# Kernel optimization log

Measured on AMD Instinct MI355X. Metric: run time of the kernel, lower is better.

## Reference

```python
import jax, jax.numpy as jnp
import numpy as np

N = 100000   # num variables
D_IN = 512
D_OUT = 512
C = 4096     # num clusters
K = 32       # vars per cluster
E = 16384    # cluster edges
S = 16       # shared vars per edge
H = 4        # num heads
NEG_SLOPE = 0.2


def setup_inputs() -> dict:
    key = jax.random.key(0)
    ks = jax.random.split(key, 8)
    xav = (6.0 / (D_IN + D_OUT)) ** 0.5  # xavier_uniform bound
    x_var = jax.random.normal(ks[0], (N, D_IN), dtype=jnp.float32)
    W_Q = jax.random.uniform(ks[1], (D_OUT, D_IN), jnp.float32, -xav, xav)
    W_K = jax.random.uniform(ks[2], (D_OUT, D_IN), jnp.float32, -xav, xav)
    W_V = jax.random.uniform(ks[3], (D_OUT, D_IN), jnp.float32, -xav, xav)
    head_weights = jnp.ones((H,), jnp.float32)
    cluster_var_ids = jax.random.randint(ks[4], (C, K), 0, N)
    cluster_edge_index = jax.random.randint(ks[5], (2, E), 0, C)
    shared_vars = jax.random.randint(ks[6], (E, S), 0, N)
    return {
        'x_var': x_var, 'W_Q': W_Q, 'W_K': W_K, 'W_V': W_V,
        'head_weights': head_weights,
        'cluster_var_ids': cluster_var_ids,
        'cluster_edge_index': cluster_edge_index,
        'shared_vars': shared_vars,
        'active_heads': 4,
    }


def reference(x_var, W_Q, W_K, W_V, head_weights,
              cluster_var_ids, cluster_edge_index, shared_vars, active_heads):
    # Per-cluster mean pooling over member variables: [C, D_in]
    cluster_feats = x_var[cluster_var_ids].mean(axis=1)
    # Linear projections (torch Linear: y = x @ W.T)
    Q = cluster_feats @ W_Q.T   # [C, D_out]
    Kc = cluster_feats @ W_K.T  # [C, D_out]
    V = cluster_feats @ W_V.T   # [C, D_out]
    c1 = cluster_edge_index[0]  # [E] source clusters
    c2 = cluster_edge_index[1]  # [E] target clusters
    # Scalar dot-product attention per cluster edge
    scale = jnp.asarray(D_OUT, jnp.float32) ** 0.5
    scores = jnp.einsum('ed,ed->e', Q[c1], Kc[c2]) / scale
    scores = jnp.where(scores >= 0, scores, NEG_SLOPE * scores)  # leaky_relu
    attn = jax.nn.sigmoid(scores) * head_weights[:active_heads].mean()  # [E]
    # Per-edge message = attn * V[c2], broadcast to each shared var of the edge
    upd = attn[:, None] * V[c2]                                   # [E, D_out]
    upd_flat = jnp.broadcast_to(upd[:, None, :], (E, S, D_OUT)).reshape(E * S, D_OUT)
    x_out = x_var.at[shared_vars.reshape(-1)].add(upd_flat)
    return x_out
```

## Files before the change

### kernel.cpp

```cpp
#include <hip/hip_runtime.h>
#include <hip/hip_bf16.h>
#include <math.h>

#define N_VARS    100000
#define D_DIM     512
#define C_CLUST   4096
#define K_VARS    32
#define E_EDGES   16384
#define S_SHARED  16
#define H_HEADS   4
#define CAP       32
#define NEG_SLOPE 0.2f

typedef __bf16 bf16x8_t __attribute__((ext_vector_type(8)));
typedef float  f32x4_t  __attribute__((ext_vector_type(4)));

__device__ __forceinline__ unsigned int f32_to_bf16_bits(float f) {
    unsigned int u = __builtin_bit_cast(unsigned int, f);
    unsigned int lsb = (u >> 16) & 1u;
    u += 0x7fffu + lsb;
    return u >> 16;
}
__device__ __forceinline__ unsigned int pack_bf16x2(float a, float b) {
    return (f32_to_bf16_bits(b) << 16) | f32_to_bf16_bits(a);
}
__device__ __forceinline__ float bf16_bits_to_f32(unsigned int h) {
    unsigned int u = h << 16;
    return __builtin_bit_cast(float, u);
}

__device__ __forceinline__ int decode_active_heads(const int* p) {
    int raw = p[0];
    if (raw >= 1 && raw <= H_HEADS) return raw;
    float f = __builtin_bit_cast(float, raw);
    if (f >= 1.0f && f <= (float)H_HEADS) return (int)f;
    return H_HEADS;
}

__global__ void convert_w_kernel(const float* __restrict__ Wq,
                                 const float* __restrict__ Wk,
                                 const float* __restrict__ Wv,
                                 unsigned int* __restrict__ Wb) {
    const float* W = (blockIdx.y == 0) ? Wq : (blockIdx.y == 1) ? Wk : Wv;
    int i = blockIdx.x * blockDim.x + threadIdx.x;
    float2 w = ((const float2*)W)[i];
    Wb[(size_t)blockIdx.y * (D_DIM * D_DIM / 2) + i] = pack_bf16x2(w.x, w.y);
}

__global__ void pool_kernel(const float* __restrict__ x,
                            const int* __restrict__ cvid,
                            uint2* __restrict__ cfb ) {
    int c = blockIdx.x * 2 + (threadIdx.x >> 7);
    int t = threadIdx.x & 127;
    float4 acc = {0.f, 0.f, 0.f, 0.f};
#pragma unroll 4
    for (int k = 0; k < K_VARS; ++k) {
        int v = cvid[c * K_VARS + k];
        float4 w = ((const float4*)(x + (size_t)v * D_DIM))[t];
        acc.x += w.x; acc.y += w.y; acc.z += w.z; acc.w += w.w;
    }
    const float inv = 1.0f / (float)K_VARS;
    uint2 o;
    o.x = pack_bf16x2(acc.x * inv, acc.y * inv);
    o.y = pack_bf16x2(acc.z * inv, acc.w * inv);
    cfb[(size_t)c * (D_DIM / 4) + t] = o;
}

__global__ __launch_bounds__(256) void gemm_kernel(
        const unsigned short* __restrict__ cfb,
        const unsigned short* __restrict__ Wb,
        float* __restrict__ Qo, float* __restrict__ Ko, float* __restrict__ Vo) {
    const unsigned short* W = Wb + (size_t)blockIdx.z * D_DIM * D_DIM;
    float* O = (blockIdx.z == 0) ? Qo : (blockIdx.z == 1) ? Ko : Vo;

    int wave = threadIdx.x >> 6;
    int lane = threadIdx.x & 63;
    int m0 = blockIdx.x * 64 + wave * 16;
    int n0 = blockIdx.y * 64;
    int mr = m0 + (lane & 15);
    int kb = (lane >> 4) * 8;

    f32x4_t acc0 = {0.f,0.f,0.f,0.f}, acc1 = {0.f,0.f,0.f,0.f};
    f32x4_t acc2 = {0.f,0.f,0.f,0.f}, acc3 = {0.f,0.f,0.f,0.f};
    const unsigned short* arow = cfb + (size_t)mr * D_DIM + kb;
    const unsigned short* b0r  = W + (size_t)(n0 +  0 + (lane & 15)) * D_DIM + kb;
    const unsigned short* b1r  = W + (size_t)(n0 + 16 + (lane & 15)) * D_DIM + kb;
    const unsigned short* b2r  = W + (size_t)(n0 + 32 + (lane & 15)) * D_DIM + kb;
    const unsigned short* b3r  = W + (size_t)(n0 + 48 + (lane & 15)) * D_DIM + kb;
#pragma unroll 4
    for (int k0 = 0; k0 < D_DIM; k0 += 32) {
        bf16x8_t a  = *(const bf16x8_t*)(arow + k0);
        bf16x8_t b0 = *(const bf16x8_t*)(b0r + k0);
        bf16x8_t b1 = *(const bf16x8_t*)(b1r + k0);
        bf16x8_t b2 = *(const bf16x8_t*)(b2r + k0);
        bf16x8_t b3 = *(const bf16x8_t*)(b3r + k0);
        acc0 = __builtin_amdgcn_mfma_f32_16x16x32_bf16(a, b0, acc0, 0, 0, 0);
        acc1 = __builtin_amdgcn_mfma_f32_16x16x32_bf16(a, b1, acc1, 0, 0, 0);
        acc2 = __builtin_amdgcn_mfma_f32_16x16x32_bf16(a, b2, acc2, 0, 0, 0);
        acc3 = __builtin_amdgcn_mfma_f32_16x16x32_bf16(a, b3, acc3, 0, 0, 0);
    }
    int rb = m0 + (lane >> 4) * 4;
    int cl = lane & 15;
#pragma unroll
    for (int r = 0; r < 4; ++r) {
        float* orow = O + (size_t)(rb + r) * D_DIM + n0 + cl;
        orow[ 0] = acc0[r];
        orow[16] = acc1[r];
        orow[32] = acc2[r];
        orow[48] = acc3[r];
    }
}

__global__ void score_kernel(const float* __restrict__ Q,
                             const float* __restrict__ Kc,
                             const int* __restrict__ cei,
                             const float* __restrict__ hw,
                             const int* __restrict__ active_heads,
                             float* __restrict__ attn) {
    int e = blockIdx.x * 4 + (threadIdx.x >> 6);
    int lane = threadIdx.x & 63;
    int c1 = cei[e];
    int c2 = cei[E_EDGES + e];
    const float4* q = (const float4*)(Q  + (size_t)c1 * D_DIM);
    const float4* k = (const float4*)(Kc + (size_t)c2 * D_DIM);
    float4 qa = q[lane], qb = q[lane + 64];
    float4 ka = k[lane], kb = k[lane + 64];
    float s = qa.x*ka.x + qa.y*ka.y + qa.z*ka.z + qa.w*ka.w
            + qb.x*kb.x + qb.y*kb.y + qb.z*kb.z + qb.w*kb.w;
#pragma unroll
    for (int off = 32; off > 0; off >>= 1)
        s += __shfl_xor(s, off);
    if (lane == 0) {
        int ah = decode_active_heads(active_heads);
        float m = 0.f;
        for (int h = 0; h < ah; ++h) m += hw[h];
        m /= (float)ah;
        float sc = s * (1.0f / sqrtf((float)D_DIM));
        sc = sc >= 0.f ? sc : NEG_SLOPE * sc;
        attn[e] = m / (1.f + __expf(-sc));
    }
}

__global__ void fill_kernel(const int* __restrict__ shared_vars,
                            const int* __restrict__ cei,
                            const float* __restrict__ attn,
                            int* __restrict__ counts,
                            unsigned int* __restrict__ bucket) {
    int j = blockIdx.x * blockDim.x + threadIdx.x;
    if (j >= E_EDGES * S_SHARED) return;
    int v = shared_vars[j];
    int e = j >> 4;
    int pos = atomicAdd(&counts[v], 1);
    if (pos < CAP) {
        unsigned int packed = (f32_to_bf16_bits(attn[e]) << 16) | (unsigned int)cei[E_EDGES + e];
        bucket[(size_t)v * CAP + pos] = packed;
    }
}

__global__ void gather_kernel(const float* __restrict__ x,
                              const float* __restrict__ V,
                              const int* __restrict__ counts,
                              const unsigned int* __restrict__ bucket,
                              float* __restrict__ out) {
    int v = blockIdx.x * 2 + (threadIdx.x >> 7);
    int t = threadIdx.x & 127;
    float4 a = ((const float4*)(x + (size_t)v * D_DIM))[t];
    int cnt = counts[v];
    if (cnt > CAP) cnt = CAP;
    const unsigned int* bk = bucket + (size_t)v * CAP;
    for (int k = 0; k < cnt; ++k) {
        unsigned int pw = bk[k];
        float at = bf16_bits_to_f32(pw >> 16);
        int c2 = pw & 0xFFFu;
        float4 vv = ((const float4*)(V + (size_t)c2 * D_DIM))[t];
        a.x += at * vv.x; a.y += at * vv.y; a.z += at * vv.z; a.w += at * vv.w;
    }
    ((float4*)(out + (size_t)v * D_DIM))[t] = a;
}

extern "C" void kernel_launch(void* const* d_in, const int* in_sizes, int n_in,
                              void* d_out, int out_size, void* d_ws, size_t ws_size,
                              hipStream_t stream) {
    const float* x_var = (const float*)d_in[0];
    const float* W_Q   = (const float*)d_in[1];
    const float* W_K   = (const float*)d_in[2];
    const float* W_V   = (const float*)d_in[3];
    const float* hw    = (const float*)d_in[4];
    const int* cvid  = (const int*)d_in[5];
    const int* cei   = (const int*)d_in[6];
    const int* shv   = (const int*)d_in[7];
    const int* ahp   = (const int*)d_in[8];

    char* ws = (char*)d_ws;
    const size_t MiB = 1024 * 1024;
    unsigned int* cfb = (unsigned int*)(ws + 0);
    unsigned int* Wb  = (unsigned int*)(ws + 4  * MiB);
    float* Q    = (float*)(ws + 6  * MiB);
    float* Kc   = (float*)(ws + 14 * MiB);
    float* V    = (float*)(ws + 22 * MiB);
    float* attn = (float*)(ws + 30 * MiB);
    int* counts = (int*)(ws + 30 * MiB + 65536);
    unsigned int* bucket = (unsigned int*)(ws + 31 * MiB);

    convert_w_kernel<<<dim3(D_DIM * D_DIM / 2 / 256, 3), 256, 0, stream>>>(
        W_Q, W_K, W_V, Wb);

    pool_kernel<<<C_CLUST / 2, 256, 0, stream>>>(x_var, cvid, (uint2*)cfb);

    gemm_kernel<<<dim3(C_CLUST / 64, D_DIM / 64, 3), 256, 0, stream>>>(
        (const unsigned short*)cfb, (const unsigned short*)Wb, Q, Kc, V);

    score_kernel<<<E_EDGES / 4, 256, 0, stream>>>(Q, Kc, cei, hw, ahp, attn);

    hipMemsetAsync(counts, 0, (size_t)N_VARS * sizeof(int), stream);
    fill_kernel<<<(E_EDGES * S_SHARED + 255) / 256, 256, 0, stream>>>(
        shv, cei, attn, counts, bucket);

    gather_kernel<<<N_VARS / 2, 256, 0, stream>>>(x_var, V, counts, bucket,
                                                  (float*)d_out);
}
```

Baseline: 530.9 us.

## Fuse score with bucket fill, zero counts in pool, widen gather per wave

Merges the score and fill kernels so each edge's attention is computed and scattered into per-variable buckets in one pass, dropping the attn buffer and one launch. The counts memset moves into the pool kernel, and the pool loop is unrolled further with a scalarised cluster index. Gather now assigns one wave per variable, loads four bucket entries at once and issues up to four V-row loads before accumulating, with nontemporal output stores. The bucket read as uint4 relies on 16-byte alignment and reads past cnt within the CAP-sized slot.

Result: faster. 495.4 us (-6.7%).

```diff
diff --git a/kernel.cpp b/kernel.cpp
--- a/kernel.cpp
+++ b/kernel.cpp
@@ -49,13 +49,19 @@
 
 __global__ void pool_kernel(const float* __restrict__ x,
                             const int* __restrict__ cvid,
-                            uint2* __restrict__ cfb ) {
+                            uint2* __restrict__ cfb ,
+                            int* __restrict__ counts) {
+    int gtid = blockIdx.x * blockDim.x + threadIdx.x;
+    if (gtid < N_VARS) counts[gtid] = 0;
+
     int c = blockIdx.x * 2 + (threadIdx.x >> 7);
+    c = __builtin_amdgcn_readfirstlane(c);
     int t = threadIdx.x & 127;
+    const int* cv = cvid + c * K_VARS;
     float4 acc = {0.f, 0.f, 0.f, 0.f};
-#pragma unroll 4
+#pragma unroll 8
     for (int k = 0; k < K_VARS; ++k) {
-        int v = cvid[c * K_VARS + k];
+        int v = cv[k];
         float4 w = ((const float4*)(x + (size_t)v * D_DIM))[t];
         acc.x += w.x; acc.y += w.y; acc.z += w.z; acc.w += w.w;
     }
@@ -111,13 +117,16 @@
     }
 }
 
-__global__ void score_kernel(const float* __restrict__ Q,
-                             const float* __restrict__ Kc,
-                             const int* __restrict__ cei,
-                             const float* __restrict__ hw,
-                             const int* __restrict__ active_heads,
-                             float* __restrict__ attn) {
-    int e = blockIdx.x * 4 + (threadIdx.x >> 6);
+__global__ __launch_bounds__(256) void score_fill_kernel(
+        const float* __restrict__ Q,
+        const float* __restrict__ Kc,
+        const int* __restrict__ cei,
+        const float* __restrict__ hw,
+        const int* __restrict__ active_heads,
+        const int* __restrict__ shared_vars,
+        int* __restrict__ counts,
+        unsigned int* __restrict__ bucket) {
+    int e = __builtin_amdgcn_readfirstlane(blockIdx.x * 4 + (threadIdx.x >> 6));
     int lane = threadIdx.x & 63;
     int c1 = cei[e];
     int c2 = cei[E_EDGES + e];
@@ -130,52 +139,62 @@
 #pragma unroll
     for (int off = 32; off > 0; off >>= 1)
         s += __shfl_xor(s, off);
-    if (lane == 0) {
-        int ah = decode_active_heads(active_heads);
-        float m = 0.f;
-        for (int h = 0; h < ah; ++h) m += hw[h];
-        m /= (float)ah;
-        float sc = s * (1.0f / sqrtf((float)D_DIM));
-        sc = sc >= 0.f ? sc : NEG_SLOPE * sc;
-        attn[e] = m / (1.f + __expf(-sc));
-    }
-}
-
-__global__ void fill_kernel(const int* __restrict__ shared_vars,
-                            const int* __restrict__ cei,
-                            const float* __restrict__ attn,
-                            int* __restrict__ counts,
-                            unsigned int* __restrict__ bucket) {
-    int j = blockIdx.x * blockDim.x + threadIdx.x;
-    if (j >= E_EDGES * S_SHARED) return;
-    int v = shared_vars[j];
-    int e = j >> 4;
-    int pos = atomicAdd(&counts[v], 1);
-    if (pos < CAP) {
-        unsigned int packed = (f32_to_bf16_bits(attn[e]) << 16) | (unsigned int)cei[E_EDGES + e];
-        bucket[(size_t)v * CAP + pos] = packed;
-    }
-}
-
-__global__ void gather_kernel(const float* __restrict__ x,
-                              const float* __restrict__ V,
-                              const int* __restrict__ counts,
-                              const unsigned int* __restrict__ bucket,
-                              float* __restrict__ out) {
-    int v = blockIdx.x * 2 + (threadIdx.x >> 7);
-    int t = threadIdx.x & 127;
-    float4 a = ((const float4*)(x + (size_t)v * D_DIM))[t];
+    int ah = decode_active_heads(active_heads);
+    float m = 0.f;
+    for (int h = 0; h < ah; ++h) m += hw[h];
+    m /= (float)ah;
+    float sc = s * (1.0f / sqrtf((float)D_DIM));
+    sc = sc >= 0.f ? sc : NEG_SLOPE * sc;
+    float attn = m / (1.f + __expf(-sc));
+    unsigned int packed = (f32_to_bf16_bits(attn) << 16) | (unsigned int)c2;
+    if (lane < S_SHARED) {
+        int v = shared_vars[e * S_SHARED + lane];
+        int pos = atomicAdd(&counts[v], 1);
+        if (pos < CAP) bucket[(size_t)v * CAP + pos] = packed;
+    }
+}
+
+__global__ __launch_bounds__(256) void gather_kernel(
+        const float* __restrict__ x,
+        const float* __restrict__ V,
+        const int* __restrict__ counts,
+        const unsigned int* __restrict__ bucket,
+        float* __restrict__ out) {
+    int v = __builtin_amdgcn_readfirstlane(blockIdx.x * 4 + (threadIdx.x >> 6));
+    int lane = threadIdx.x & 63;
+    const f32x4_t* xr = (const f32x4_t*)(x + (size_t)v * D_DIM);
+    f32x4_t a0 = xr[lane];
+    f32x4_t a1 = xr[lane + 64];
     int cnt = counts[v];
     if (cnt > CAP) cnt = CAP;
     const unsigned int* bk = bucket + (size_t)v * CAP;
-    for (int k = 0; k < cnt; ++k) {
-        unsigned int pw = bk[k];
-        float at = bf16_bits_to_f32(pw >> 16);
-        int c2 = pw & 0xFFFu;
-        float4 vv = ((const float4*)(V + (size_t)c2 * D_DIM))[t];
-        a.x += at * vv.x; a.y += at * vv.y; a.z += at * vv.z; a.w += at * vv.w;
-    }
-    ((float4*)(out + (size_t)v * D_DIM))[t] = a;
+    for (int k = 0; k < cnt; k += 4) {
+        uint4 pw = *(const uint4*)(bk + k);
+        int m = cnt - k;
+        const f32x4_t* r0 = (const f32x4_t*)(V + (size_t)(pw.x & 0xFFFu) * D_DIM);
+        f32x4_t u0a = r0[lane], u0b = r0[lane + 64];
+        f32x4_t u1a, u1b, u2a, u2b, u3a, u3b;
+        if (m > 1) {
+            const f32x4_t* r1 = (const f32x4_t*)(V + (size_t)(pw.y & 0xFFFu) * D_DIM);
+            u1a = r1[lane]; u1b = r1[lane + 64];
+        }
+        if (m > 2) {
+            const f32x4_t* r2 = (const f32x4_t*)(V + (size_t)(pw.z & 0xFFFu) * D_DIM);
+            u2a = r2[lane]; u2b = r2[lane + 64];
+        }
+        if (m > 3) {
+            const f32x4_t* r3 = (const f32x4_t*)(V + (size_t)(pw.w & 0xFFFu) * D_DIM);
+            u3a = r3[lane]; u3b = r3[lane + 64];
+        }
+        float t0 = bf16_bits_to_f32(pw.x >> 16);
+        a0 += t0 * u0a; a1 += t0 * u0b;
+        if (m > 1) { float t1 = bf16_bits_to_f32(pw.y >> 16); a0 += t1 * u1a; a1 += t1 * u1b; }
+        if (m > 2) { float t2 = bf16_bits_to_f32(pw.z >> 16); a0 += t2 * u2a; a1 += t2 * u2b; }
+        if (m > 3) { float t3 = bf16_bits_to_f32(pw.w >> 16); a0 += t3 * u3a; a1 += t3 * u3b; }
+    }
+    f32x4_t* orow = (f32x4_t*)(out + (size_t)v * D_DIM);
+    __builtin_nontemporal_store(a0, orow + lane);
+    __builtin_nontemporal_store(a1, orow + lane + 64);
 }
 
 extern "C" void kernel_launch(void* const* d_in, const int* in_sizes, int n_in,
@@ -198,24 +217,20 @@
     float* Q    = (float*)(ws + 6  * MiB);
     float* Kc   = (float*)(ws + 14 * MiB);
     float* V    = (float*)(ws + 22 * MiB);
-    float* attn = (float*)(ws + 30 * MiB);
     int* counts = (int*)(ws + 30 * MiB + 65536);
     unsigned int* bucket = (unsigned int*)(ws + 31 * MiB);
 
     convert_w_kernel<<<dim3(D_DIM * D_DIM / 2 / 256, 3), 256, 0, stream>>>(
         W_Q, W_K, W_V, Wb);
 
-    pool_kernel<<<C_CLUST / 2, 256, 0, stream>>>(x_var, cvid, (uint2*)cfb);
+    pool_kernel<<<C_CLUST / 2, 256, 0, stream>>>(x_var, cvid, (uint2*)cfb, counts);
 
     gemm_kernel<<<dim3(C_CLUST / 64, D_DIM / 64, 3), 256, 0, stream>>>(
         (const unsigned short*)cfb, (const unsigned short*)Wb, Q, Kc, V);
 
-    score_kernel<<<E_EDGES / 4, 256, 0, stream>>>(Q, Kc, cei, hw, ahp, attn);
-
-    hipMemsetAsync(counts, 0, (size_t)N_VARS * sizeof(int), stream);
-    fill_kernel<<<(E_EDGES * S_SHARED + 255) / 256, 256, 0, stream>>>(
-        shv, cei, attn, counts, bucket);
-
-    gather_kernel<<<N_VARS / 2, 256, 0, stream>>>(x_var, V, counts, bucket,
+    score_fill_kernel<<<E_EDGES / 4, 256, 0, stream>>>(
+        Q, Kc, cei, hw, ahp, shv, counts, bucket);
+
+    gather_kernel<<<N_VARS / 4, 256, 0, stream>>>(x_var, V, counts, bucket,
                                                   (float*)d_out);
 }
```
